# Kernel optimization log

Hardware: AMD Instinct MI355X
Metric: run time of the kernel (lower is better)

Reference implementation:

```python
import jax, jax.numpy as jnp
import numpy as np

N = 8192   # nodes
F = 128    # features
ORDER = 4  # polynomial taps


def setup_inputs() -> dict:
    key = jax.random.key(0)
    k1, k2, k3 = jax.random.split(key, 3)
    X = jax.random.normal(k1, (N, F), dtype=jnp.float32)
    # scale GSO so powers don't blow up (spectral-norm-ish normalization)
    S = jax.random.normal(k2, (N, N), dtype=jnp.float32) / jnp.sqrt(jnp.float32(N))
    coefficients = jax.random.uniform(k3, (ORDER,), dtype=jnp.float32)
    return {"X": X, "S": S, "coefficients": coefficients}


def reference(X, S, coefficients):
    # y = sum_{k=0}^{K-1} h_k * S^k X
    Z = X
    y = coefficients[0] * Z
    for k in range(1, ORDER):  # small fixed tap count; loop over taps, not data
        Z = S @ Z              # S^k X, [N, F]
        y = y + coefficients[k] * Z
    return y
```

## Files before the change

### kernel.cpp

```cpp
#include <hip/hip_runtime.h>
#include <hip/hip_bf16.h>
#include <stdint.h>


typedef __attribute__((ext_vector_type(8))) short     bf16x8;
typedef __attribute__((ext_vector_type(8))) uint16_t  u16x8;
typedef __attribute__((ext_vector_type(4))) float     f32x4;

#define NN 8192
#define NF 128
#define ZSTRIDE (8192 + 64)

#define WAITV(n) asm volatile("s_waitcnt vmcnt(" #n ")" ::: "memory")
#define WAITL0   asm volatile("s_waitcnt lgkmcnt(0)" ::: "memory")

__device__ inline uint16_t f2bf(float f) {
    uint32_t u = __builtin_bit_cast(uint32_t, f);
    u += 0x7fffu + ((u >> 16) & 1u);
    return (uint16_t)(u >> 16);
}

__device__ inline void gl2lds16(const void* g, uint8_t* l) {
    __builtin_amdgcn_global_load_lds(
        (const __attribute__((address_space(1))) uint32_t*)g,
        (__attribute__((address_space(3))) uint32_t*)l,
        16, 0, 0);
}

__device__ inline bf16x8 ld16(const uint8_t* p) {
    return __builtin_bit_cast(bf16x8, *(const u16x8*)p);
}

__global__ __launch_bounds__(256) void k_convert(const float* __restrict__ S,
                                                 uint16_t* __restrict__ S16) {
    const size_t n8 = (size_t)NN * NN / 8;
    const size_t stride = (size_t)gridDim.x * 256;
    for (size_t i = (size_t)blockIdx.x * 256 + threadIdx.x; i < n8; i += stride) {
        f32x4 a = __builtin_nontemporal_load((const f32x4*)(S + i * 8));
        f32x4 b = __builtin_nontemporal_load((const f32x4*)(S + i * 8 + 4));
        u16x8 p;
#pragma unroll
        for (int j = 0; j < 4; ++j) { p[j] = f2bf(a[j]); p[j + 4] = f2bf(b[j]); }
        *(u16x8*)(S16 + i * 8) = p;
    }
}

__global__ __launch_bounds__(256) void k_prep(const float* __restrict__ X,
                                              const float* __restrict__ coeff,
                                              float* __restrict__ y,
                                              uint16_t* __restrict__ ZT0) {
    __shared__ float tile[16][NF + 4];
    const int t  = threadIdx.x;
    const int r0 = blockIdx.x * 16;
    const float h0 = coeff[0];
#pragma unroll
    for (int i = 0; i < 2; ++i) {
        int o   = (i * 256 + t) * 4;
        int row = o >> 7, col = o & 127;
        f32x4 v = *(const f32x4*)(X + (size_t)(r0 + row) * NF + col);
        *(f32x4*)&tile[row][col] = v;
        *(f32x4*)(y + (size_t)(r0 + row) * NF + col) = v * h0;
    }
    __syncthreads();
    const int c = t >> 1, rh = t & 1;
    u16x8 pk;
#pragma unroll
    for (int e = 0; e < 8; ++e) pk[e] = f2bf(tile[rh * 8 + e][c]);
    *(u16x8*)(ZT0 + (size_t)c * ZSTRIDE + r0 + rh * 8) = pk;
}

template<int KS>
__global__ __launch_bounds__(512, 4) void k_gemm_bf(
    const uint16_t* __restrict__ S16, const uint16_t* __restrict__ ZTin,
    float* __restrict__ P)
{
    __shared__ __align__(16) uint8_t smem[3][24576];
    const int t = threadIdx.x, lane = t & 63;
    const int w = t >> 6, m = lane & 15, g = lane >> 4;
    const int rt = w & 3, ch = w >> 2;
    const int mt = blockIdx.x & 127, ks = blockIdx.x >> 7;
    const int r0 = mt * 64;
    const int kb = ks * (NN / KS);
    constexpr int NT = (NN / KS) / 64;

    const int srow = t >> 3, sc = t & 7;
    const int scs  = (sc ^ (srow & 7)) << 3;
    const uint16_t* asrc = S16  + (size_t)(r0 + srow) * NN + kb + scs;
    const uint16_t* bsrc = ZTin + (size_t)srow * ZSTRIDE   + kb + scs;

    const int sw   = m & 7;
    const int aoff = (rt * 16 + m) * 128 + ((g ^ sw) << 4);
    const int bof  = 8192 + (ch * 64 + m) * 128 + ((g ^ sw) << 4);

    f32x4 acc[4] = {};

    auto stage = [&](int buf, int kt) {
        const int ko = kt * 64;
        uint8_t* b = smem[buf];
        gl2lds16(asrc + ko, b + t * 16);
        gl2lds16(bsrc + ko, b + 8192 + t * 16);
        gl2lds16(bsrc + (size_t)64 * ZSTRIDE + ko, b + 16384 + t * 16);
    };

    stage(0, 0);
    stage(1, 1);
    int cur = 0;
#pragma unroll 1
    for (int kt = 0; kt < NT; ++kt) {
        if (kt + 2 < NT) {
            int nxt = cur + 2; if (nxt >= 3) nxt -= 3;
            stage(nxt, kt + 2);
            WAITV(6);
        } else if (kt + 2 == NT) {
            WAITV(3);
        } else {
            WAITV(0);
        }
        __builtin_amdgcn_s_barrier();
        __builtin_amdgcn_sched_barrier(0);
        const uint8_t* bb = smem[cur];
        bf16x8 a0 = ld16(bb + aoff);
        bf16x8 a1 = ld16(bb + (aoff ^ 64));
#pragma unroll
        for (int ct = 0; ct < 4; ++ct) {
            acc[ct] = __builtin_amdgcn_mfma_f32_16x16x32_bf16(
                a0, ld16(bb + bof + ct * 16 * 128), acc[ct], 0, 0, 0);
            acc[ct] = __builtin_amdgcn_mfma_f32_16x16x32_bf16(
                a1, ld16(bb + ((bof + ct * 16 * 128) ^ 64)), acc[ct], 0, 0, 0);
        }
        WAITL0;
        __builtin_amdgcn_sched_barrier(0);
        __builtin_amdgcn_s_barrier();
        cur = (cur + 1 == 3) ? 0 : cur + 1;
    }

    float* pb = P + ((size_t)ks * NN + r0 + rt * 16 + 4 * g) * NF + ch * 64 + m;
#pragma unroll
    for (int ct = 0; ct < 4; ++ct)
#pragma unroll
        for (int i = 0; i < 4; ++i)
            pb[(size_t)i * NF + ct * 16] = acc[ct][i];
}

template<int KS, bool WRITE_ZT>
__global__ __launch_bounds__(256) void k_combine(const float* __restrict__ P,
                                                 float* __restrict__ y,
                                                 uint16_t* __restrict__ ZTout,
                                                 const float* __restrict__ coeff,
                                                 int pass) {
    __shared__ float tile[16][NF + 4];
    const int t = threadIdx.x, r0 = blockIdx.x * 16;
    const float hk = coeff[pass];
    const int row = t >> 4, col = (t & 15) * 8;
    const size_t off = (size_t)(r0 + row) * NF + col;
    f32x4 s0 = *(const f32x4*)(P + off);
    f32x4 s1 = *(const f32x4*)(P + off + 4);
#pragma unroll
    for (int k = 1; k < KS; ++k) {
        s0 += *(const f32x4*)(P + (size_t)k * NN * NF + off);
        s1 += *(const f32x4*)(P + (size_t)k * NN * NF + off + 4);
    }
    float* yp = y + off;
    f32x4 y0 = *(const f32x4*)yp, y1 = *(const f32x4*)(yp + 4);
    *(f32x4*)yp       = y0 + hk * s0;
    *(f32x4*)(yp + 4) = y1 + hk * s1;
    if (WRITE_ZT) {
        *(f32x4*)&tile[row][col]     = s0;
        *(f32x4*)&tile[row][col + 4] = s1;
        __syncthreads();
        const int c = t >> 1, rh = t & 1;
        u16x8 pk;
#pragma unroll
        for (int e = 0; e < 8; ++e) pk[e] = f2bf(tile[rh * 8 + e][c]);
        *(u16x8*)(ZTout + (size_t)c * ZSTRIDE + r0 + rh * 8) = pk;
    }
}

template<int KS>
static void run(const float* X, const float* S, const float* coeff, float* y,
                uint16_t* ZT0, uint16_t* ZT1, uint16_t* S16, float* P,
                hipStream_t stream) {
    k_prep<<<dim3(512), dim3(256), 0, stream>>>(X, coeff, y, ZT0);
    k_convert<<<dim3(2048), dim3(256), 0, stream>>>(S, S16);
    k_gemm_bf<KS><<<dim3(128 * KS), dim3(512), 0, stream>>>(S16, ZT0, P);
    k_combine<KS, true ><<<dim3(512), dim3(256), 0, stream>>>(P, y, ZT1, coeff, 1);
    k_gemm_bf<KS><<<dim3(128 * KS), dim3(512), 0, stream>>>(S16, ZT1, P);
    k_combine<KS, true ><<<dim3(512), dim3(256), 0, stream>>>(P, y, ZT0, coeff, 2);
    k_gemm_bf<KS><<<dim3(128 * KS), dim3(512), 0, stream>>>(S16, ZT0, P);
    k_combine<KS, false><<<dim3(512), dim3(256), 0, stream>>>(P, y, nullptr, coeff, 3);
}

extern "C" void kernel_launch(void* const* d_in, const int* in_sizes, int n_in,
                              void* d_out, int out_size, void* d_ws, size_t ws_size,
                              hipStream_t stream) {
    const float* X     = (const float*)d_in[0];
    const float* S     = (const float*)d_in[1];
    const float* coeff = (const float*)d_in[2];
    float* y = (float*)d_out;

    uint8_t* ws = (uint8_t*)d_ws;
    const size_t zb     = ((size_t)NF * ZSTRIDE * sizeof(uint16_t) + 255) & ~(size_t)255;
    const size_t s16b   = (size_t)NN * NN * sizeof(uint16_t);
    const size_t base   = 2 * zb + s16b;
    const size_t pslice = (size_t)NN * NF * sizeof(float);
    uint16_t* ZT0 = (uint16_t*)ws;
    uint16_t* ZT1 = (uint16_t*)(ws + zb);
    uint16_t* S16 = (uint16_t*)(ws + 2 * zb);
    float*    P   = (float*)(ws + base);

    if (ws_size >= base + 4 * pslice)
        run<4>(X, S, coeff, y, ZT0, ZT1, S16, P, stream);
    else if (ws_size >= base + 2 * pslice)
        run<2>(X, S, coeff, y, ZT0, ZT1, S16, P, stream);
    else
        run<1>(X, S, coeff, y, ZT0, ZT1, S16, P, stream);
}
```

Measured before the change: 187.0 us.

## Fuse prep into convert kernel, double-buffer GEMM, add split-K of eight

```diff
diff --git a/kernel.cpp b/kernel.cpp
--- a/kernel.cpp
+++ b/kernel.cpp
@@ -31,11 +31,39 @@
     return __builtin_bit_cast(bf16x8, *(const u16x8*)p);
 }
 
-__global__ __launch_bounds__(256) void k_convert(const float* __restrict__ S,
-                                                 uint16_t* __restrict__ S16) {
-    const size_t n8 = (size_t)NN * NN / 8;
+__global__ __launch_bounds__(256) void k_cvprep(const float* __restrict__ S,
+                                                uint16_t* __restrict__ S16,
+                                                const float* __restrict__ X,
+                                                const float* __restrict__ coeff,
+                                                float* __restrict__ y,
+                                                uint16_t* __restrict__ ZT0) {
+    __shared__ float tile[16][NF + 4];
+    const int t = threadIdx.x, bx = blockIdx.x;
+
+    if (bx < 512) {
+        const int r0 = bx * 16;
+        const float h0 = coeff[0];
+#pragma unroll
+        for (int i = 0; i < 2; ++i) {
+            int o   = (i * 256 + t) * 4;
+            int row = o >> 7, col = o & 127;
+            f32x4 v = *(const f32x4*)(X + (size_t)(r0 + row) * NF + col);
+            *(f32x4*)&tile[row][col] = v;
+            *(f32x4*)(y + (size_t)(r0 + row) * NF + col) = v * h0;
+        }
+        __syncthreads();
+        const int c = t >> 1, rh = t & 1;
+        u16x8 pk;
+#pragma unroll
+        for (int e = 0; e < 8; ++e) pk[e] = f2bf(tile[rh * 8 + e][c]);
+        *(u16x8*)(ZT0 + (size_t)c * ZSTRIDE + r0 + rh * 8) = pk;
+    }
+
+    const size_t base = (size_t)bx * 256 + t;
     const size_t stride = (size_t)gridDim.x * 256;
-    for (size_t i = (size_t)blockIdx.x * 256 + threadIdx.x; i < n8; i += stride) {
+#pragma unroll 4
+    for (int it = 0; it < 16; ++it) {
+        size_t i = base + (size_t)it * stride;
         f32x4 a = __builtin_nontemporal_load((const f32x4*)(S + i * 8));
         f32x4 b = __builtin_nontemporal_load((const f32x4*)(S + i * 8 + 4));
         u16x8 p;
@@ -45,80 +73,30 @@
     }
 }
 
-__global__ __launch_bounds__(256) void k_prep(const float* __restrict__ X,
-                                              const float* __restrict__ coeff,
-                                              float* __restrict__ y,
-                                              uint16_t* __restrict__ ZT0) {
-    __shared__ float tile[16][NF + 4];
-    const int t  = threadIdx.x;
-    const int r0 = blockIdx.x * 16;
-    const float h0 = coeff[0];
-#pragma unroll
-    for (int i = 0; i < 2; ++i) {
-        int o   = (i * 256 + t) * 4;
-        int row = o >> 7, col = o & 127;
-        f32x4 v = *(const f32x4*)(X + (size_t)(r0 + row) * NF + col);
-        *(f32x4*)&tile[row][col] = v;
-        *(f32x4*)(y + (size_t)(r0 + row) * NF + col) = v * h0;
-    }
-    __syncthreads();
-    const int c = t >> 1, rh = t & 1;
-    u16x8 pk;
-#pragma unroll
-    for (int e = 0; e < 8; ++e) pk[e] = f2bf(tile[rh * 8 + e][c]);
-    *(u16x8*)(ZT0 + (size_t)c * ZSTRIDE + r0 + rh * 8) = pk;
-}
-
-template<int KS>
-__global__ __launch_bounds__(512, 4) void k_gemm_bf(
-    const uint16_t* __restrict__ S16, const uint16_t* __restrict__ ZTin,
-    float* __restrict__ P)
-{
-    __shared__ __align__(16) uint8_t smem[3][24576];
-    const int t = threadIdx.x, lane = t & 63;
-    const int w = t >> 6, m = lane & 15, g = lane >> 4;
-    const int rt = w & 3, ch = w >> 2;
-    const int mt = blockIdx.x & 127, ks = blockIdx.x >> 7;
-    const int r0 = mt * 64;
-    const int kb = ks * (NN / KS);
-    constexpr int NT = (NN / KS) / 64;
-
-    const int srow = t >> 3, sc = t & 7;
-    const int scs  = (sc ^ (srow & 7)) << 3;
-    const uint16_t* asrc = S16  + (size_t)(r0 + srow) * NN + kb + scs;
-    const uint16_t* bsrc = ZTin + (size_t)srow * ZSTRIDE   + kb + scs;
-
-    const int sw   = m & 7;
-    const int aoff = (rt * 16 + m) * 128 + ((g ^ sw) << 4);
-    const int bof  = 8192 + (ch * 64 + m) * 128 + ((g ^ sw) << 4);
-
-    f32x4 acc[4] = {};
-
+template<int NT>
+__device__ inline void gemm_core(const uint16_t* asrc, const uint16_t* bsrc,
+                                 uint8_t* smem, int t, f32x4 (&acc)[4],
+                                 int aoff, int bof) {
     auto stage = [&](int buf, int kt) {
         const int ko = kt * 64;
-        uint8_t* b = smem[buf];
+        uint8_t* b = smem + buf * 24576;
         gl2lds16(asrc + ko, b + t * 16);
         gl2lds16(bsrc + ko, b + 8192 + t * 16);
         gl2lds16(bsrc + (size_t)64 * ZSTRIDE + ko, b + 16384 + t * 16);
     };
-
     stage(0, 0);
-    stage(1, 1);
     int cur = 0;
 #pragma unroll 1
     for (int kt = 0; kt < NT; ++kt) {
-        if (kt + 2 < NT) {
-            int nxt = cur + 2; if (nxt >= 3) nxt -= 3;
-            stage(nxt, kt + 2);
-            WAITV(6);
-        } else if (kt + 2 == NT) {
+        if (kt + 1 < NT) {
+            stage(cur ^ 1, kt + 1);
             WAITV(3);
         } else {
             WAITV(0);
         }
         __builtin_amdgcn_s_barrier();
         __builtin_amdgcn_sched_barrier(0);
-        const uint8_t* bb = smem[cur];
+        const uint8_t* bb = smem + cur * 24576;
         bf16x8 a0 = ld16(bb + aoff);
         bf16x8 a1 = ld16(bb + (aoff ^ 64));
 #pragma unroll
@@ -131,8 +109,35 @@
         WAITL0;
         __builtin_amdgcn_sched_barrier(0);
         __builtin_amdgcn_s_barrier();
-        cur = (cur + 1 == 3) ? 0 : cur + 1;
-    }
+        cur ^= 1;
+    }
+}
+
+template<int KS>
+__global__ __launch_bounds__(512, 4) void k_gemm_bf(
+    const uint16_t* __restrict__ S16, const uint16_t* __restrict__ ZTin,
+    float* __restrict__ P)
+{
+    __shared__ __align__(16) uint8_t smem[2][24576];
+    const int t = threadIdx.x, lane = t & 63;
+    const int w = t >> 6, m = lane & 15, g = lane >> 4;
+    const int rt = w & 3, ch = w >> 2;
+    const int mt = blockIdx.x & 127, ks = blockIdx.x >> 7;
+    const int r0 = mt * 64;
+    const int kb = ks * (NN / KS);
+    constexpr int NT = (NN / KS) / 64;
+
+    const int srow = t >> 3, sc = t & 7;
+    const int scs  = (sc ^ (srow & 7)) << 3;
+    const uint16_t* asrc = S16  + (size_t)(r0 + srow) * NN + kb + scs;
+    const uint16_t* bsrc = ZTin + (size_t)srow * ZSTRIDE   + kb + scs;
+
+    const int sw   = m & 7;
+    const int aoff = (rt * 16 + m) * 128 + ((g ^ sw) << 4);
+    const int bof  = 8192 + (ch * 64 + m) * 128 + ((g ^ sw) << 4);
+
+    f32x4 acc[4] = {};
+    gemm_core<NT>(asrc, bsrc, &smem[0][0], t, acc, aoff, bof);
 
     float* pb = P + ((size_t)ks * NN + r0 + rt * 16 + 4 * g) * NF + ch * 64 + m;
 #pragma unroll
@@ -180,8 +185,7 @@
 static void run(const float* X, const float* S, const float* coeff, float* y,
                 uint16_t* ZT0, uint16_t* ZT1, uint16_t* S16, float* P,
                 hipStream_t stream) {
-    k_prep<<<dim3(512), dim3(256), 0, stream>>>(X, coeff, y, ZT0);
-    k_convert<<<dim3(2048), dim3(256), 0, stream>>>(S, S16);
+    k_cvprep<<<dim3(2048), dim3(256), 0, stream>>>(S, S16, X, coeff, y, ZT0);
     k_gemm_bf<KS><<<dim3(128 * KS), dim3(512), 0, stream>>>(S16, ZT0, P);
     k_combine<KS, true ><<<dim3(512), dim3(256), 0, stream>>>(P, y, ZT1, coeff, 1);
     k_gemm_bf<KS><<<dim3(128 * KS), dim3(512), 0, stream>>>(S16, ZT1, P);
@@ -208,7 +212,9 @@
     uint16_t* S16 = (uint16_t*)(ws + 2 * zb);
     float*    P   = (float*)(ws + base);
 
-    if (ws_size >= base + 4 * pslice)
+    if (ws_size >= base + 8 * pslice)
+        run<8>(X, S, coeff, y, ZT0, ZT1, S16, P, stream);
+    else if (ws_size >= base + 4 * pslice)
         run<4>(X, S, coeff, y, ZT0, ZT1, S16, P, stream);
     else if (ws_size >= base + 2 * pslice)
         run<2>(X, S, coeff, y, ZT0, ZT1, S16, P, stream);
```

Result: slower. 196.5 us (+5.0%).
